# Kernel optimization log

Measured on AMD Instinct MI355X. Metric: run time of the kernel, lower is better.

## Reference

```python
import jax, jax.numpy as jnp
import numpy as np

B_IMG, P, C, H, W = 32, 2, 128, 56, 56
b = B_IMG * P * P


def setup_inputs() -> dict:
    key = jax.random.key(0)
    ks = jax.random.split(key, 9)
    inp = {"x": jax.random.normal(ks[0], (b, C, H, W), dtype=jnp.float32)}
    names = ["topW", "botW", "leftW", "rightW", "topleftW", "toprightW", "botleftW", "botrightW"]
    for i, n in enumerate(names):
        inp[n] = jax.random.uniform(ks[i + 1], (C,), dtype=jnp.float32)
    inp["padding"] = 1
    inp["num_patches"] = P
    return inp


def reference(x, topW, botW, leftW, rightW, topleftW, toprightW, botleftW, botrightW, padding, num_patches):
    # padding is fixed to 1 (the 2-wide boundary convs emit exactly 1 row/col).
    bb, Cc, Hh, Ww = x.shape
    Pn = num_patches
    # Depthwise boundary "convs": per-channel weighted sum of the 2 boundary rows/cols.
    top_pad = topW[None, :, None] * (x[:, :, 0, :] + x[:, :, 1, :])          # [b,C,W]
    bot_pad = botW[None, :, None] * (x[:, :, Hh - 2, :] + x[:, :, Hh - 1, :])  # [b,C,W]
    left_pad = leftW[None, :, None] * (x[:, :, :, 0] + x[:, :, :, 1])        # [b,C,H]
    right_pad = rightW[None, :, None] * (x[:, :, :, Ww - 2] + x[:, :, :, Ww - 1])  # [b,C,H]

    y = jnp.pad(x, ((0, 0), (0, 0), (1, 1), (1, 1)))  # [b,C,H+2,W+2]
    y = y.at[:, :, 0, 1:Ww + 1].set(top_pad)
    y = y.at[:, :, Hh + 1, 1:Ww + 1].set(bot_pad)
    y = y.at[:, :, 1:Hh + 1, 0].set(left_pad)
    y = y.at[:, :, 1:Hh + 1, Ww + 1].set(right_pad)
    # Corners: padded[1,1]==x[0,0] etc. are untouched by the edge writes.
    y = y.at[:, :, 0, 0].set(topleftW[None, :] * x[:, :, 0, 0])
    y = y.at[:, :, 0, Ww + 1].set(toprightW[None, :] * x[:, :, 0, Ww - 1])
    y = y.at[:, :, Hh + 1, 0].set(botleftW[None, :] * x[:, :, Hh - 1, 0])
    y = y.at[:, :, Hh + 1, Ww + 1].set(botrightW[None, :] * x[:, :, Hh - 1, Ww - 1])

    # Patch-boundary zeroing masks (patches at the true image border get zero pad).
    idx = jnp.arange(bb)
    within = idx % (Pn * Pn)
    top_m = within < Pn
    bot_m = within >= Pn * Pn - Pn
    left_m = (idx % Pn) == 0
    right_m = (idx % Pn) == Pn - 1
    rows = jnp.arange(Hh + 2)
    cols = jnp.arange(Ww + 2)
    zero = ((top_m[:, None, None] & (rows == 0)[None, :, None])
            | (bot_m[:, None, None] & (rows == Hh + 1)[None, :, None])
            | (left_m[:, None, None] & (cols == 0)[None, None, :])
            | (right_m[:, None, None] & (cols == Ww + 1)[None, None, :]))  # [b,H+2,W+2]
    return jnp.where(zero[:, None, :, :], jnp.zeros((), x.dtype), y)
```

## Files before the change

### kernel.cpp

```cpp
#include <hip/hip_runtime.h>

constexpr int B  = 128;
constexpr int C  = 128;
constexpr int H  = 56, W = 56;
constexpr int HO = H + 2, WO = W + 2;
constexpr int PLANE_IN  = H * W;
constexpr int PLANE_OUT = HO * WO;

__global__ __launch_bounds__(256) void pad2d_kernel(
    const float* __restrict__ x,
    const float* __restrict__ topW, const float* __restrict__ botW,
    const float* __restrict__ leftW, const float* __restrict__ rightW,
    const float* __restrict__ tlW,  const float* __restrict__ trW,
    const float* __restrict__ blW,  const float* __restrict__ brW,
    const int* __restrict__ np_ptr,
    float* __restrict__ out)
{
    const int plane = blockIdx.x;
    const int b   = plane / C;
    const int c   = plane - b * C;
    const int tid = threadIdx.x;

    const int Pn = *np_ptr;
    const int within = b % (Pn * Pn);
    const bool top_z   = within < Pn;
    const bool bot_z   = within >= Pn * Pn - Pn;
    const bool left_z  = (b % Pn) == 0;
    const bool right_z = (b % Pn) == Pn - 1;

    const float* __restrict__ xin = x + (size_t)plane * PLANE_IN;
    float* __restrict__ o = out + (size_t)plane * PLANE_OUT;

    const float4* __restrict__ x4 = (const float4*)xin;
    constexpr int NV = H * (W / 4);
    for (int i = tid; i < NV; i += 256) {
        const int r = i / 14;
        const int q = i - r * 14;
        const float4 v = x4[i];
        float* dst = o + (r + 1) * WO + 1 + q * 4;
        dst[0] = v.x; dst[1] = v.y; dst[2] = v.z; dst[3] = v.w;
    }

    if (tid < 228) {
        if (tid < 56) {
            const int col = tid;
            const float v = top_z ? 0.f
                : topW[c] * (xin[col] + xin[W + col]);
            o[col + 1] = v;
        } else if (tid < 112) {
            const int col = tid - 56;
            const float v = bot_z ? 0.f
                : botW[c] * (xin[(H - 2) * W + col] + xin[(H - 1) * W + col]);
            o[(HO - 1) * WO + col + 1] = v;
        } else if (tid < 168) {
            const int r = tid - 112;
            const float v = left_z ? 0.f
                : leftW[c] * (xin[r * W] + xin[r * W + 1]);
            o[(r + 1) * WO] = v;
        } else if (tid < 224) {
            const int r = tid - 168;
            const float v = right_z ? 0.f
                : rightW[c] * (xin[r * W + W - 2] + xin[r * W + W - 1]);
            o[(r + 1) * WO + WO - 1] = v;
        } else if (tid == 224) {
            o[0] = (top_z || left_z) ? 0.f : tlW[c] * xin[0];
        } else if (tid == 225) {
            o[WO - 1] = (top_z || right_z) ? 0.f : trW[c] * xin[W - 1];
        } else if (tid == 226) {
            o[(HO - 1) * WO] = (bot_z || left_z) ? 0.f : blW[c] * xin[(H - 1) * W];
        } else {
            o[(HO - 1) * WO + WO - 1] =
                (bot_z || right_z) ? 0.f : brW[c] * xin[(H - 1) * W + W - 1];
        }
    }
}

extern "C" void kernel_launch(void* const* d_in, const int* in_sizes, int n_in,
                              void* d_out, int out_size, void* d_ws, size_t ws_size,
                              hipStream_t stream) {
    const float* x      = (const float*)d_in[0];
    const float* topW   = (const float*)d_in[1];
    const float* botW   = (const float*)d_in[2];
    const float* leftW  = (const float*)d_in[3];
    const float* rightW = (const float*)d_in[4];
    const float* tlW    = (const float*)d_in[5];
    const float* trW    = (const float*)d_in[6];
    const float* blW    = (const float*)d_in[7];
    const float* brW    = (const float*)d_in[8];
    const int* np_ptr   = (const int*)d_in[10];
    float* out = (float*)d_out;

    pad2d_kernel<<<dim3(B * C), dim3(256), 0, stream>>>(
        x, topW, botW, leftW, rightW, tlW, trW, blW, brW, np_ptr, out);
}
```

Before: 399.2 us.

## Split padding into row-per-thread interior kernel and separate border kernel

Replaces the one-block-per-plane kernel with two kernels. The interior kernel assigns one thread per output row, loads the 56-float input row into registers, computes the left and right pad values inline, and writes the full 58-wide row with aligned float4 stores chosen by row parity. A second small kernel writes the top and bottom border rows, including corners. The aim is to replace scalar unaligned stores with vectorized ones and drop the separate edge pass over the interior, at the cost of an extra launch, heavy register use per thread, and strided per-thread access across rows.

```diff
diff --git a/kernel.cpp b/kernel.cpp
--- a/kernel.cpp
+++ b/kernel.cpp
@@ -6,20 +6,79 @@
 constexpr int HO = H + 2, WO = W + 2;
 constexpr int PLANE_IN  = H * W;
 constexpr int PLANE_OUT = HO * WO;
+constexpr int NPLANES   = B * C;
+constexpr int NROWS     = NPLANES * H;
 
-__global__ __launch_bounds__(256) void pad2d_kernel(
+__global__ __launch_bounds__(256) void pad_interior(
+    const float* __restrict__ x,
+    const float* __restrict__ leftW, const float* __restrict__ rightW,
+    const int* __restrict__ np_ptr,
+    float* __restrict__ out)
+{
+    const int t     = blockIdx.x * 256 + threadIdx.x;
+    const int plane = t / H;
+    const int r     = t - plane * H;
+    const int b     = plane >> 7;
+    const int c     = plane & (C - 1);
+
+    const int Pn = *np_ptr;
+    const bool left_z  = (b % Pn) == 0;
+    const bool right_z = (b % Pn) == Pn - 1;
+
+    const float* __restrict__ xin = x + (size_t)plane * PLANE_IN + r * W;
+    const float4* __restrict__ x4 = (const float4*)xin;
+
+    float v[56];
+    #pragma unroll
+    for (int k = 0; k < 14; ++k) {
+        float4 q = x4[k];
+        v[4*k] = q.x; v[4*k+1] = q.y; v[4*k+2] = q.z; v[4*k+3] = q.w;
+    }
+
+    const float lp = left_z  ? 0.f : leftW[c]  * (v[0]  + v[1]);
+    const float rp = right_z ? 0.f : rightW[c] * (v[54] + v[55]);
+
+    float* __restrict__ po = out + (size_t)plane * PLANE_OUT + (r + 1) * WO;
+    if (r & 1) {
+        float4* p4 = (float4*)po;
+        float4 s; s.x = lp; s.y = v[0]; s.z = v[1]; s.w = v[2];
+        p4[0] = s;
+        #pragma unroll
+        for (int k = 1; k < 14; ++k) {
+            float4 u; u.x = v[4*k-1]; u.y = v[4*k]; u.z = v[4*k+1]; u.w = v[4*k+2];
+            p4[k] = u;
+        }
+        po[56] = v[55]; po[57] = rp;
+    } else {
+        po[0] = lp; po[1] = v[0];
+        float4* p4 = (float4*)(po + 2);
+        #pragma unroll
+        for (int k = 0; k < 13; ++k) {
+            float4 u; u.x = v[4*k+1]; u.y = v[4*k+2]; u.z = v[4*k+3]; u.w = v[4*k+4];
+            p4[k] = u;
+        }
+        float4 u; u.x = v[53]; u.y = v[54]; u.z = v[55]; u.w = rp;
+        p4[13] = u;
+    }
+}
+
+__global__ __launch_bounds__(256) void pad_border(
     const float* __restrict__ x,
     const float* __restrict__ topW, const float* __restrict__ botW,
-    const float* __restrict__ leftW, const float* __restrict__ rightW,
     const float* __restrict__ tlW,  const float* __restrict__ trW,
     const float* __restrict__ blW,  const float* __restrict__ brW,
     const int* __restrict__ np_ptr,
     float* __restrict__ out)
 {
-    const int plane = blockIdx.x;
-    const int b   = plane / C;
-    const int c   = plane - b * C;
-    const int tid = threadIdx.x;
+    const int t  = blockIdx.x * 256 + threadIdx.x;
+    const int j  = t & 63;
+    const int pr = t >> 6;
+    if (j >= WO) return;
+
+    const int plane  = pr >> 1;
+    const bool isTop = (pr & 1) == 0;
+    const int b = plane >> 7;
+    const int c = plane & (C - 1);
 
     const int Pn = *np_ptr;
     const int within = b % (Pn * Pn);
@@ -29,50 +88,19 @@
     const bool right_z = (b % Pn) == Pn - 1;
 
     const float* __restrict__ xin = x + (size_t)plane * PLANE_IN;
-    float* __restrict__ o = out + (size_t)plane * PLANE_OUT;
+    float* __restrict__ po = out + (size_t)plane * PLANE_OUT + (isTop ? 0 : (HO - 1) * WO);
 
-    const float4* __restrict__ x4 = (const float4*)xin;
-    constexpr int NV = H * (W / 4);
-    for (int i = tid; i < NV; i += 256) {
-        const int r = i / 14;
-        const int q = i - r * 14;
-        const float4 v = x4[i];
-        float* dst = o + (r + 1) * WO + 1 + q * 4;
-        dst[0] = v.x; dst[1] = v.y; dst[2] = v.z; dst[3] = v.w;
+    float val;
+    if (isTop) {
+        if (j == 0)            val = (top_z || left_z)  ? 0.f : tlW[c] * xin[0];
+        else if (j == WO - 1)  val = (top_z || right_z) ? 0.f : trW[c] * xin[W - 1];
+        else                   val = top_z ? 0.f : topW[c] * (xin[j - 1] + xin[W + j - 1]);
+    } else {
+        if (j == 0)            val = (bot_z || left_z)  ? 0.f : blW[c] * xin[(H - 1) * W];
+        else if (j == WO - 1)  val = (bot_z || right_z) ? 0.f : brW[c] * xin[(H - 1) * W + W - 1];
+        else                   val = bot_z ? 0.f : botW[c] * (xin[(H - 2) * W + j - 1] + xin[(H - 1) * W + j - 1]);
     }
-
-    if (tid < 228) {
-        if (tid < 56) {
-            const int col = tid;
-            const float v = top_z ? 0.f
-                : topW[c] * (xin[col] + xin[W + col]);
-            o[col + 1] = v;
-        } else if (tid < 112) {
-            const int col = tid - 56;
-            const float v = bot_z ? 0.f
-                : botW[c] * (xin[(H - 2) * W + col] + xin[(H - 1) * W + col]);
-            o[(HO - 1) * WO + col + 1] = v;
-        } else if (tid < 168) {
-            const int r = tid - 112;
-            const float v = left_z ? 0.f
-                : leftW[c] * (xin[r * W] + xin[r * W + 1]);
-            o[(r + 1) * WO] = v;
-        } else if (tid < 224) {
-            const int r = tid - 168;
-            const float v = right_z ? 0.f
-                : rightW[c] * (xin[r * W + W - 2] + xin[r * W + W - 1]);
-            o[(r + 1) * WO + WO - 1] = v;
-        } else if (tid == 224) {
-            o[0] = (top_z || left_z) ? 0.f : tlW[c] * xin[0];
-        } else if (tid == 225) {
-            o[WO - 1] = (top_z || right_z) ? 0.f : trW[c] * xin[W - 1];
-        } else if (tid == 226) {
-            o[(HO - 1) * WO] = (bot_z || left_z) ? 0.f : blW[c] * xin[(H - 1) * W];
-        } else {
-            o[(HO - 1) * WO + WO - 1] =
-                (bot_z || right_z) ? 0.f : brW[c] * xin[(H - 1) * W + W - 1];
-        }
-    }
+    po[j] = val;
 }
 
 extern "C" void kernel_launch(void* const* d_in, const int* in_sizes, int n_in,
@@ -90,6 +118,8 @@
     const int* np_ptr   = (const int*)d_in[10];
     float* out = (float*)d_out;
 
-    pad2d_kernel<<<dim3(B * C), dim3(256), 0, stream>>>(
-        x, topW, botW, leftW, rightW, tlW, trW, blW, brW, np_ptr, out);
+    pad_interior<<<dim3(NROWS / 256), dim3(256), 0, stream>>>(
+        x, leftW, rightW, np_ptr, out);
+    pad_border<<<dim3(2 * NPLANES * 64 / 256), dim3(256), 0, stream>>>(
+        x, topW, botW, tlW, trW, blW, brW, np_ptr, out);
 }
```

Result: slower. 419.0 us (+5.0%).
